# Optimization experiments

Measured on AMD Instinct MI355X. Metric: run time of the kernel, lower is better.

The kernel has to match this reference:

```python
import jax, jax.numpy as jnp
import numpy as np

N_NODES = 100000
N_EDGES = 1600000
IN_DIM, HID_DIM, OUT_DIM = 128, 128, 64


def setup_inputs() -> dict:
    key = jax.random.key(0)
    k1, k2, k3, k4 = jax.random.split(key, 4)
    x = jax.random.normal(k1, (N_NODES, IN_DIM), dtype=jnp.float32)
    edge_index = jax.random.randint(k2, (2, N_EDGES), 0, N_NODES, dtype=jnp.int64)
    W1 = jax.random.normal(k3, (IN_DIM, HID_DIM), dtype=jnp.float32) * (1.0 / np.sqrt(IN_DIM))
    b1 = jnp.zeros((HID_DIM,), dtype=jnp.float32)
    W2 = jax.random.normal(k4, (HID_DIM, OUT_DIM), dtype=jnp.float32) * (1.0 / np.sqrt(HID_DIM))
    b2 = jnp.zeros((OUT_DIM,), dtype=jnp.float32)
    return {"x": x, "edge_index": edge_index, "W1": W1, "b1": b1, "W2": W2, "b2": b2}


def _gcn_conv(x, W, b, src, dst, num_nodes):
    # PyG GCNConv (normalize=True): h = D^{-1/2} A_hat D^{-1/2} (x W) + b
    h = x @ W  # [N, out]
    ones = jnp.ones(src.shape[0], dtype=h.dtype)
    deg = jax.ops.segment_sum(ones, dst, num_segments=num_nodes)  # in-degree incl self-loops
    dinv = jnp.where(deg > 0, jax.lax.rsqrt(deg), jnp.zeros_like(deg))
    norm = dinv[src] * dinv[dst]  # [E]
    msg = h[src] * norm[:, None]  # gather + scale, [E, out]
    out = jax.ops.segment_sum(msg, dst, num_segments=num_nodes)  # scatter-add
    return out + b


def reference(x, edge_index, W1, b1, W2, b2):
    n = x.shape[0]
    loop = jnp.arange(n, dtype=edge_index.dtype)
    src = jnp.concatenate([edge_index[0], loop])  # add_self_loops=True
    dst = jnp.concatenate([edge_index[1], loop])
    h = jax.nn.elu(_gcn_conv(x, W1, b1, src, dst, n))
    out = jax.nn.elu(_gcn_conv(h, W2, b2, src, dst, n))
    return out
```

## Files before the change

kernel.cpp:

```cpp
#include <hip/hip_runtime.h>
#include <hip/hip_bf16.h>

#define N_NODES 100000
#define N_EDGES 1600000
#define IN_DIM  128
#define HID_DIM 128
#define OUT_DIM 64

#define BKT_BITS 9
#define BKT_SIZE 512
#define NBUCK    ((N_NODES + BKT_SIZE - 1) / BKT_SIZE)
#define BCAP     8768
#define EPB      2048
#define NTILE    8

typedef __attribute__((ext_vector_type(8))) short short8;
typedef __attribute__((ext_vector_type(4))) float floatx4;

__device__ __forceinline__ float eluf(float x) { return x > 0.0f ? x : expm1f(x); }
__device__ __forceinline__ unsigned short bfbits(float f) {
    union { __hip_bfloat16 h; unsigned short u; } c; c.h = __float2bfloat16(f); return c.u;
}
__device__ __forceinline__ unsigned packbf(float a, float b) {
    return (unsigned)bfbits(a) | ((unsigned)bfbits(b) << 16);
}
__device__ __forceinline__ float lo16(unsigned u) { return __uint_as_float(u << 16); }
__device__ __forceinline__ float hi16(unsigned u) { return __uint_as_float(u & 0xffff0000u); }
__device__ __forceinline__ unsigned tile_of(unsigned src) { return (src * 8u) / 100000u; }

__device__ __forceinline__ int esrc(const int* ei, int e, int is64) {
    return is64 ? ei[2 * e] : ei[e];
}
__device__ __forceinline__ int edst(const int* ei, int e, int is64) {
    return is64 ? ei[2 * (N_EDGES + e)] : ei[N_EDGES + e];
}

__global__ void k_init(const int* __restrict__ ei, int* __restrict__ flag,
                       int* __restrict__ cursor) {
    __shared__ int acc;
    if (threadIdx.x == 0) acc = 0;
    __syncthreads();
    int v = 0;
    for (int e = threadIdx.x; e < 1024; e += 256) v |= ei[2 * e + 1];
    atomicOr(&acc, v);
    __syncthreads();
    if (threadIdx.x == 0) flag[0] = (acc == 0) ? 1 : 0;
    if (threadIdx.x < NBUCK) cursor[threadIdx.x] = 0;
}

__launch_bounds__(256)
__global__ void k_bucket(const int* __restrict__ ei, const int* __restrict__ flag,
                         int* __restrict__ cursor, unsigned* __restrict__ eb) {
    __shared__ int hist[NBUCK];
    __shared__ int base[NBUCK];
    int t = threadIdx.x;
    int is64 = flag[0];
    int e0 = blockIdx.x * EPB;
    int s[8], d[8];
#pragma unroll
    for (int q = 0; q < 8; q++) {
        int e = e0 + q * 256 + t;
        if (e < N_EDGES) { s[q] = esrc(ei, e, is64); d[q] = edst(ei, e, is64); }
        else d[q] = -1;
    }
    for (int i = t; i < NBUCK; i += 256) hist[i] = 0;
    __syncthreads();
#pragma unroll
    for (int q = 0; q < 8; q++)
        if (d[q] >= 0) atomicAdd(&hist[d[q] >> BKT_BITS], 1);
    __syncthreads();
    for (int i = t; i < NBUCK; i += 256) {
        int h = hist[i];
        base[i] = (h > 0) ? atomicAdd(&cursor[i], h) : 0;
    }
    __syncthreads();
#pragma unroll
    for (int q = 0; q < 8; q++)
        if (d[q] >= 0) {
            int bk = d[q] >> BKT_BITS;
            int p = atomicAdd(&base[bk], 1);
            if (p < BCAP)
                eb[bk * BCAP + p] = ((unsigned)s[q] << BKT_BITS) | (unsigned)(d[q] & (BKT_SIZE - 1));
        }
}

__launch_bounds__(256)
__global__ void k_csr(const int* __restrict__ cursor, unsigned* __restrict__ eb,
                      unsigned short* __restrict__ row16, unsigned char* __restrict__ deg8,
                      float* __restrict__ dinv) {
    __shared__ unsigned stage[BCAP];
    __shared__ int bins[BKT_SIZE * NTILE];
    __shared__ int sc[256];
    int t = threadIdx.x, b = blockIdx.x;
    int cbeg = b * BCAP;
    int count = cursor[b];
    if (count > BCAP) count = BCAP;
    for (int i = t; i < BKT_SIZE * NTILE; i += 256) bins[i] = 0;
    __syncthreads();
    for (int i = t; i < count; i += 256) {
        unsigned e = eb[cbeg + i];
        stage[i] = e;
        unsigned key = ((e & (BKT_SIZE - 1)) << 3) + tile_of(e >> BKT_BITS);
        atomicAdd(&bins[key], 1);
    }
    __syncthreads();
    int loc[16];
    int s = 0;
#pragma unroll
    for (int i = 0; i < 16; i++) { loc[i] = bins[t * 16 + i]; s += loc[i]; }
    sc[t] = s;
    __syncthreads();
    int acc = s;
    for (int off = 1; off < 256; off <<= 1) {
        int v = (t >= off) ? sc[t - off] : 0;
        __syncthreads();
        acc += v; sc[t] = acc;
        __syncthreads();
    }
    int run = acc - s;
#pragma unroll
    for (int i = 0; i < 16; i++) { bins[t * 16 + i] = run; run += loc[i]; }
    __syncthreads();
    int nbase = b * BKT_SIZE;
    for (int i = t; i < BKT_SIZE; i += 256) {
        int n = nbase + i;
        if (n < N_NODES) {
            int st = bins[i << 3];
            int en = (i == BKT_SIZE - 1) ? count : bins[(i + 1) << 3];
            row16[n] = (unsigned short)st;
            deg8[n] = (unsigned char)(en - st);
            dinv[n] = rsqrtf((float)(en - st) + 1.0f);
        }
    }
    __syncthreads();
    for (int i = t; i < count; i += 256) {
        unsigned e = stage[i];
        unsigned src = e >> BKT_BITS;
        unsigned key = ((e & (BKT_SIZE - 1)) << 3) + tile_of(src);
        int p = atomicAdd(&bins[key], 1);
        eb[cbeg + p] = src;
    }
}

__global__ void k_cast_scale(const float4* __restrict__ x4, const float* __restrict__ dinv,
                             uint2* __restrict__ xbs) {
    int i = blockIdx.x * blockDim.x + threadIdx.x;
    if (i >= N_NODES * (IN_DIM / 4)) return;
    float dd = dinv[i >> 5];
    float4 v = x4[i];
    uint2 o = { packbf(v.x * dd, v.y * dd), packbf(v.z * dd, v.w * dd) };
    xbs[i] = o;
}

__launch_bounds__(256)
__global__ void k_gather1(const unsigned* __restrict__ xbs, const float* __restrict__ dinv,
                          const unsigned short* __restrict__ row16,
                          const unsigned char* __restrict__ deg8,
                          const unsigned* __restrict__ csr, unsigned* __restrict__ agg) {
    int w = (blockIdx.x * blockDim.x + threadIdx.x) >> 6;
    int lane = threadIdx.x & 63;
    if (w >= N_NODES) return;
    int beg = (w >> BKT_BITS) * BCAP + row16[w];
    int dg = deg8[w];
    beg = __builtin_amdgcn_readfirstlane(beg);
    int end = beg + __builtin_amdgcn_readfirstlane(dg);
    float dd = dinv[w];
    unsigned sv = xbs[w * 64 + lane];
    float a0 = lo16(sv), a1 = hi16(sv);
    int j = beg;
    for (; j + 8 <= end; j += 8) {
        int s[8]; unsigned u[8];
#pragma unroll
        for (int q = 0; q < 8; q++) s[q] = (int)csr[j + q];
#pragma unroll
        for (int q = 0; q < 8; q++) u[q] = xbs[s[q] * 64 + lane];
#pragma unroll
        for (int q = 0; q < 8; q++) { a0 += lo16(u[q]); a1 += hi16(u[q]); }
    }
    if (j + 4 <= end) {
        int s[4]; unsigned u[4];
#pragma unroll
        for (int q = 0; q < 4; q++) s[q] = (int)csr[j + q];
#pragma unroll
        for (int q = 0; q < 4; q++) u[q] = xbs[s[q] * 64 + lane];
#pragma unroll
        for (int q = 0; q < 4; q++) { a0 += lo16(u[q]); a1 += hi16(u[q]); }
        j += 4;
    }
    if (j + 2 <= end) {
        int s0 = (int)csr[j], s1 = (int)csr[j + 1];
        unsigned u0 = xbs[s0 * 64 + lane], u1 = xbs[s1 * 64 + lane];
        a0 += lo16(u0) + lo16(u1); a1 += hi16(u0) + hi16(u1);
        j += 2;
    }
    if (j < end) {
        unsigned u0 = xbs[(int)csr[j] * 64 + lane];
        a0 += lo16(u0); a1 += hi16(u0);
    }
    agg[w * 64 + lane] = packbf(a0 * dd, a1 * dd);
}

__launch_bounds__(256)
__global__ void k_gather2(const unsigned* __restrict__ h2s, const float* __restrict__ dinv,
                          const unsigned short* __restrict__ row16,
                          const unsigned char* __restrict__ deg8,
                          const unsigned* __restrict__ csr,
                          const float* __restrict__ b2, float2* __restrict__ out) {
    int w = (blockIdx.x * blockDim.x + threadIdx.x) >> 6;
    int lane = threadIdx.x & 63;
    if (w >= N_NODES) return;
    int half = lane >> 5, p = lane & 31;
    int beg = (w >> BKT_BITS) * BCAP + row16[w];
    int dg = deg8[w];
    beg = __builtin_amdgcn_readfirstlane(beg);
    int end = beg + __builtin_amdgcn_readfirstlane(dg);
    float dd = dinv[w];
    unsigned sv = h2s[w * 32 + p];
    float a0 = half ? 0.0f : lo16(sv);
    float a1 = half ? 0.0f : hi16(sv);
    int j = beg;
    for (; j + 8 <= end; j += 8) {
        int s[8]; unsigned u[4];
#pragma unroll
        for (int q = 0; q < 8; q++) s[q] = (int)csr[j + q];
#pragma unroll
        for (int i = 0; i < 4; i++) u[i] = h2s[s[2 * i + half] * 32 + p];
#pragma unroll
        for (int i = 0; i < 4; i++) { a0 += lo16(u[i]); a1 += hi16(u[i]); }
    }
    if (j + 4 <= end) {
        int s[4];
#pragma unroll
        for (int q = 0; q < 4; q++) s[q] = (int)csr[j + q];
        unsigned u0 = h2s[s[half] * 32 + p];
        unsigned u1 = h2s[s[2 + half] * 32 + p];
        a0 += lo16(u0) + lo16(u1); a1 += hi16(u0) + hi16(u1);
        j += 4;
    }
    if (j + 2 <= end) {
        int s0 = (int)csr[j], s1 = (int)csr[j + 1];
        unsigned u = h2s[(half ? s1 : s0) * 32 + p];
        a0 += lo16(u); a1 += hi16(u);
        j += 2;
    }
    if (j < end && !half) {
        unsigned u = h2s[(int)csr[j] * 32 + p];
        a0 += lo16(u); a1 += hi16(u);
    }
    a0 += __shfl_xor(a0, 32);
    a1 += __shfl_xor(a1, 32);
    if (!half) {
        float2 bias = *(const float2*)(b2 + 2 * p);
        float2 r = { eluf(a0 * dd + bias.x), eluf(a1 * dd + bias.y) };
        out[w * 32 + p] = r;
    }
}

__launch_bounds__(256)
__global__ void k_gemm1_mfma(unsigned* __restrict__ agg, const float* __restrict__ W1,
                             const float* __restrict__ b1, int nblk) {
    __shared__ short w1p[4][8][64][8];
    int t = threadIdx.x;
    for (int idx = t; idx < 8192; idx += 256) {
        int j2 = idx & 3, l = (idx >> 2) & 63, ct = (idx >> 8) & 7, kk = idx >> 11;
        int k = kk * 32 + (l >> 4) * 8 + j2 * 2;
        int c = ct * 16 + (l & 15);
        ((unsigned*)w1p)[idx] = packbf(W1[k * HID_DIM + c], W1[(k + 1) * HID_DIM + c]);
    }
    int lane = t & 63, wave = t >> 6;
    int q = lane >> 4, m = lane & 15;
    floatx4 bias[8];
#pragma unroll
    for (int ct = 0; ct < 8; ct++) bias[ct] = *(const floatx4*)(b1 + ct * 16 + q * 4);
    __syncthreads();
    for (int blk = blockIdx.x * 4 + wave; blk < nblk; blk += gridDim.x * 4) {
        int r = blk * 16 + m;
        const short8* arow = (const short8*)(agg + r * 64);
        short8 bfr[4];
#pragma unroll
        for (int kk = 0; kk < 4; kk++) bfr[kk] = arow[kk * 4 + q];
        floatx4 acc[8];
#pragma unroll
        for (int ct = 0; ct < 8; ct++) acc[ct] = (floatx4)0.0f;
#pragma unroll
        for (int kk = 0; kk < 4; kk++)
#pragma unroll
            for (int ct = 0; ct < 8; ct++) {
                short8 af = *(const short8*)(&w1p[kk][ct][lane][0]);
                acc[ct] = __builtin_amdgcn_mfma_f32_16x16x32_bf16(af, bfr[kk], acc[ct], 0, 0, 0);
            }
        unsigned* hrow = agg + r * 64;
#pragma unroll
        for (int ct = 0; ct < 8; ct++) {
            uint2 o;
            o.x = packbf(eluf(acc[ct][0] + bias[ct][0]), eluf(acc[ct][1] + bias[ct][1]));
            o.y = packbf(eluf(acc[ct][2] + bias[ct][2]), eluf(acc[ct][3] + bias[ct][3]));
            *(uint2*)(hrow + ct * 8 + q * 2) = o;
        }
    }
}

__launch_bounds__(256)
__global__ void k_gemm2_mfma(const unsigned* __restrict__ h1, const float* __restrict__ W2,
                             const float* __restrict__ dinv, unsigned* __restrict__ h2s,
                             int nblk) {
    __shared__ short w2p[4][4][64][8];
    int t = threadIdx.x;
    for (int idx = t; idx < 4096; idx += 256) {
        int j2 = idx & 3, l = (idx >> 2) & 63, ct = (idx >> 8) & 3, kk = idx >> 10;
        int k = kk * 32 + (l >> 4) * 8 + j2 * 2;
        int c = ct * 16 + (l & 15);
        ((unsigned*)w2p)[idx] = packbf(W2[k * OUT_DIM + c], W2[(k + 1) * OUT_DIM + c]);
    }
    int lane = t & 63, wave = t >> 6;
    int q = lane >> 4, m = lane & 15;
    __syncthreads();
    for (int blk = blockIdx.x * 4 + wave; blk < nblk; blk += gridDim.x * 4) {
        int r = blk * 16 + m;
        const short8* arow = (const short8*)(h1 + r * 64);
        short8 bfr[4];
#pragma unroll
        for (int kk = 0; kk < 4; kk++) bfr[kk] = arow[kk * 4 + q];
        floatx4 acc[4];
#pragma unroll
        for (int ct = 0; ct < 4; ct++) acc[ct] = (floatx4)0.0f;
#pragma unroll
        for (int kk = 0; kk < 4; kk++)
#pragma unroll
            for (int ct = 0; ct < 4; ct++) {
                short8 af = *(const short8*)(&w2p[kk][ct][lane][0]);
                acc[ct] = __builtin_amdgcn_mfma_f32_16x16x32_bf16(af, bfr[kk], acc[ct], 0, 0, 0);
            }
        float ddr = dinv[r];
        unsigned* orow = h2s + r * 32;
#pragma unroll
        for (int ct = 0; ct < 4; ct++) {
            uint2 o;
            o.x = packbf(acc[ct][0] * ddr, acc[ct][1] * ddr);
            o.y = packbf(acc[ct][2] * ddr, acc[ct][3] * ddr);
            *(uint2*)(orow + ct * 8 + q * 2) = o;
        }
    }
}

extern "C" void kernel_launch(void* const* d_in, const int* in_sizes, int n_in,
                              void* d_out, int out_size, void* d_ws, size_t ws_size,
                              hipStream_t stream) {
    const float* x  = (const float*)d_in[0];
    const int*   ei = (const int*)d_in[1];
    const float* W1 = (const float*)d_in[2];
    const float* b1 = (const float*)d_in[3];
    const float* W2 = (const float*)d_in[4];
    const float* b2 = (const float*)d_in[5];

    const size_t OFF_FLAG  = 0;
    const size_t OFF_CUR   = 16;
    const size_t OFF_ROW16 = 272;
    const size_t OFF_DEG8  = 50272;
    const size_t OFF_DINV  = 75272;
    const size_t OFF_EB    = 175272;
    const size_t OFF_XB    = 1893800;
    const size_t OFF_AGG   = 8293800;
    const size_t needed = (OFF_AGG + 6400000) * 4;
    if (ws_size < needed) return;

    int*            flag   = (int*)d_ws + OFF_FLAG;
    int*            cursor = (int*)d_ws + OFF_CUR;
    unsigned short* row16  = (unsigned short*)((int*)d_ws + OFF_ROW16);
    unsigned char*  deg8   = (unsigned char*)((int*)d_ws + OFF_DEG8);
    float*          dinv   = (float*)d_ws + OFF_DINV;
    unsigned*       eb     = (unsigned*)d_ws + OFF_EB;
    unsigned*       xbs    = (unsigned*)d_ws + OFF_XB;
    unsigned*       agg    = (unsigned*)d_ws + OFF_AGG;

    k_init<<<1, 256, 0, stream>>>(ei, flag, cursor);
    k_bucket<<<(N_EDGES + EPB - 1) / EPB, 256, 0, stream>>>(ei, flag, cursor, eb);
    k_csr<<<NBUCK, 256, 0, stream>>>(cursor, eb, row16, deg8, dinv);

    k_cast_scale<<<(N_NODES * (IN_DIM / 4) + 255) / 256, 256, 0, stream>>>(
        (const float4*)x, dinv, (uint2*)xbs);

    k_gather1<<<(N_NODES * 64 + 255) / 256, 256, 0, stream>>>(
        xbs, dinv, row16, deg8, eb, agg);
    k_gemm1_mfma<<<1024, 256, 0, stream>>>(agg, W1, b1, N_NODES / 16);

    k_gemm2_mfma<<<1024, 256, 0, stream>>>(agg, W2, dinv, xbs, N_NODES / 16);
    k_gather2<<<(N_NODES * 64 + 255) / 256, 256, 0, stream>>>(
        xbs, dinv, row16, deg8, eb, b2, (float2*)d_out);
}
```

Before: 327.2 us.

## Tile-synchronised multi-node gather, fuse both GEMMs, prepack weights once

```diff
diff --git a/kernel.cpp b/kernel.cpp
--- a/kernel.cpp
+++ b/kernel.cpp
@@ -14,6 +14,9 @@
 #define EPB      2048
 #define NTILE    8
 
+#define G1B 1536
+#define NPW 17
+
 typedef __attribute__((ext_vector_type(8))) short short8;
 typedef __attribute__((ext_vector_type(4))) float floatx4;
 
@@ -36,16 +39,37 @@
 }
 
 __global__ void k_init(const int* __restrict__ ei, int* __restrict__ flag,
-                       int* __restrict__ cursor) {
+                       int* __restrict__ cursor, const float* __restrict__ W1,
+                       const float* __restrict__ W2, unsigned* __restrict__ w1q,
+                       unsigned* __restrict__ w2q) {
+    int t = threadIdx.x;
+    if (blockIdx.x == 1) {
+        for (int idx = t; idx < 8192; idx += 256) {
+            int j2 = idx & 3, l = (idx >> 2) & 63, ct = (idx >> 8) & 7, kk = idx >> 11;
+            int k = kk * 32 + (l >> 4) * 8 + j2 * 2;
+            int c = ct * 16 + (l & 15);
+            w1q[idx] = packbf(W1[k * HID_DIM + c], W1[(k + 1) * HID_DIM + c]);
+        }
+        return;
+    }
+    if (blockIdx.x == 2) {
+        for (int idx = t; idx < 4096; idx += 256) {
+            int j2 = idx & 3, l = (idx >> 2) & 63, ct = (idx >> 8) & 3, kk = idx >> 10;
+            int k = kk * 32 + (l >> 4) * 8 + j2 * 2;
+            int c = ct * 16 + (l & 15);
+            w2q[idx] = packbf(W2[k * OUT_DIM + c], W2[(k + 1) * OUT_DIM + c]);
+        }
+        return;
+    }
     __shared__ int acc;
-    if (threadIdx.x == 0) acc = 0;
+    if (t == 0) acc = 0;
     __syncthreads();
     int v = 0;
-    for (int e = threadIdx.x; e < 1024; e += 256) v |= ei[2 * e + 1];
+    for (int e = t; e < 1024; e += 256) v |= ei[2 * e + 1];
     atomicOr(&acc, v);
     __syncthreads();
-    if (threadIdx.x == 0) flag[0] = (acc == 0) ? 1 : 0;
-    if (threadIdx.x < NBUCK) cursor[threadIdx.x] = 0;
+    if (t == 0) flag[0] = (acc == 0) ? 1 : 0;
+    if (t < NBUCK) cursor[t] = 0;
 }
 
 __launch_bounds__(256)
@@ -87,7 +111,7 @@
 __launch_bounds__(256)
 __global__ void k_csr(const int* __restrict__ cursor, unsigned* __restrict__ eb,
                       unsigned short* __restrict__ row16, unsigned char* __restrict__ deg8,
-                      float* __restrict__ dinv) {
+                      float* __restrict__ dinv, unsigned short* __restrict__ ts16) {
     __shared__ unsigned stage[BCAP];
     __shared__ int bins[BKT_SIZE * NTILE];
     __shared__ int sc[256];
@@ -130,6 +154,12 @@
             row16[n] = (unsigned short)st;
             deg8[n] = (unsigned char)(en - st);
             dinv[n] = rsqrtf((float)(en - st) + 1.0f);
+            uint4 o;
+            o.x = (unsigned)bins[i * 8 + 0] | ((unsigned)bins[i * 8 + 1] << 16);
+            o.y = (unsigned)bins[i * 8 + 2] | ((unsigned)bins[i * 8 + 3] << 16);
+            o.z = (unsigned)bins[i * 8 + 4] | ((unsigned)bins[i * 8 + 5] << 16);
+            o.w = (unsigned)bins[i * 8 + 6] | ((unsigned)bins[i * 8 + 7] << 16);
+            ((uint4*)ts16)[n] = o;
         }
     }
     __syncthreads();
@@ -152,52 +182,138 @@
     xbs[i] = o;
 }
 
+__launch_bounds__(256, 6)
+__global__ void k_gather1_ts(const unsigned* __restrict__ xbs,
+                             const float* __restrict__ dinv,
+                             const unsigned char* __restrict__ deg8,
+                             const unsigned short* __restrict__ ts16,
+                             const unsigned* __restrict__ csr,
+                             unsigned* __restrict__ agg) {
+    int tid = threadIdx.x;
+    int wid = __builtin_amdgcn_readfirstlane((int)(blockIdx.x * 256 + tid) >> 6);
+    int lane = tid & 63;
+    int n0 = wid * NPW;
+    float a0[NPW], a1[NPW];
+#pragma unroll
+    for (int i = 0; i < NPW; i++) { a0[i] = 0.0f; a1[i] = 0.0f; }
+    for (int t = 0; t < 8; t++) {
+#pragma unroll
+        for (int i = 0; i < NPW; i++) {
+            int n = n0 + i;
+            if (n < N_NODES) {
+                int bb = (n >> BKT_BITS) * BCAP;
+                int a = bb + (int)ts16[n * 8 + t];
+                int b = (t < 7) ? bb + (int)ts16[n * 8 + t + 1]
+                                : bb + (int)ts16[n * 8] + (int)deg8[n];
+                a = __builtin_amdgcn_readfirstlane(a);
+                b = __builtin_amdgcn_readfirstlane(b);
+                if ((int)tile_of((unsigned)n) == t) {
+                    unsigned u = xbs[n * 64 + lane];
+                    a0[i] += lo16(u); a1[i] += hi16(u);
+                }
+                while (a + 4 <= b) {
+                    int s0 = __builtin_amdgcn_readfirstlane((int)csr[a]);
+                    int s1 = __builtin_amdgcn_readfirstlane((int)csr[a + 1]);
+                    int s2 = __builtin_amdgcn_readfirstlane((int)csr[a + 2]);
+                    int s3 = __builtin_amdgcn_readfirstlane((int)csr[a + 3]);
+                    unsigned u0 = xbs[s0 * 64 + lane], u1 = xbs[s1 * 64 + lane];
+                    unsigned u2 = xbs[s2 * 64 + lane], u3 = xbs[s3 * 64 + lane];
+                    a0[i] += lo16(u0) + lo16(u1) + lo16(u2) + lo16(u3);
+                    a1[i] += hi16(u0) + hi16(u1) + hi16(u2) + hi16(u3);
+                    a += 4;
+                }
+                if (a + 2 <= b) {
+                    int s0 = __builtin_amdgcn_readfirstlane((int)csr[a]);
+                    int s1 = __builtin_amdgcn_readfirstlane((int)csr[a + 1]);
+                    unsigned u0 = xbs[s0 * 64 + lane], u1 = xbs[s1 * 64 + lane];
+                    a0[i] += lo16(u0) + lo16(u1);
+                    a1[i] += hi16(u0) + hi16(u1);
+                    a += 2;
+                }
+                if (a < b) {
+                    int s0 = __builtin_amdgcn_readfirstlane((int)csr[a]);
+                    unsigned u0 = xbs[s0 * 64 + lane];
+                    a0[i] += lo16(u0); a1[i] += hi16(u0);
+                }
+            }
+        }
+        __syncthreads();
+    }
+#pragma unroll
+    for (int i = 0; i < NPW; i++) {
+        int n = n0 + i;
+        if (n < N_NODES) {
+            float dd = dinv[n];
+            agg[n * 64 + lane] = packbf(a0[i] * dd, a1[i] * dd);
+        }
+    }
+}
+
 __launch_bounds__(256)
-__global__ void k_gather1(const unsigned* __restrict__ xbs, const float* __restrict__ dinv,
-                          const unsigned short* __restrict__ row16,
-                          const unsigned char* __restrict__ deg8,
-                          const unsigned* __restrict__ csr, unsigned* __restrict__ agg) {
-    int w = (blockIdx.x * blockDim.x + threadIdx.x) >> 6;
-    int lane = threadIdx.x & 63;
-    if (w >= N_NODES) return;
-    int beg = (w >> BKT_BITS) * BCAP + row16[w];
-    int dg = deg8[w];
-    beg = __builtin_amdgcn_readfirstlane(beg);
-    int end = beg + __builtin_amdgcn_readfirstlane(dg);
-    float dd = dinv[w];
-    unsigned sv = xbs[w * 64 + lane];
-    float a0 = lo16(sv), a1 = hi16(sv);
-    int j = beg;
-    for (; j + 8 <= end; j += 8) {
-        int s[8]; unsigned u[8];
-#pragma unroll
-        for (int q = 0; q < 8; q++) s[q] = (int)csr[j + q];
-#pragma unroll
-        for (int q = 0; q < 8; q++) u[q] = xbs[s[q] * 64 + lane];
-#pragma unroll
-        for (int q = 0; q < 8; q++) { a0 += lo16(u[q]); a1 += hi16(u[q]); }
-    }
-    if (j + 4 <= end) {
-        int s[4]; unsigned u[4];
-#pragma unroll
-        for (int q = 0; q < 4; q++) s[q] = (int)csr[j + q];
-#pragma unroll
-        for (int q = 0; q < 4; q++) u[q] = xbs[s[q] * 64 + lane];
-#pragma unroll
-        for (int q = 0; q < 4; q++) { a0 += lo16(u[q]); a1 += hi16(u[q]); }
-        j += 4;
-    }
-    if (j + 2 <= end) {
-        int s0 = (int)csr[j], s1 = (int)csr[j + 1];
-        unsigned u0 = xbs[s0 * 64 + lane], u1 = xbs[s1 * 64 + lane];
-        a0 += lo16(u0) + lo16(u1); a1 += hi16(u0) + hi16(u1);
-        j += 2;
-    }
-    if (j < end) {
-        unsigned u0 = xbs[(int)csr[j] * 64 + lane];
-        a0 += lo16(u0); a1 += hi16(u0);
-    }
-    agg[w * 64 + lane] = packbf(a0 * dd, a1 * dd);
+__global__ void k_gemm12(const unsigned* __restrict__ agg, const unsigned* __restrict__ w1q,
+                         const unsigned* __restrict__ w2q, const float* __restrict__ b1,
+                         const float* __restrict__ dinv, unsigned* __restrict__ h2s,
+                         int nblk) {
+    __shared__ unsigned w1p[8192];
+    __shared__ unsigned w2p[4096];
+    __shared__ unsigned h1s[4][16 * 68 + 4];
+    int t = threadIdx.x;
+    for (int i = t; i < 8192; i += 256) w1p[i] = w1q[i];
+    for (int i = t; i < 4096; i += 256) w2p[i] = w2q[i];
+    int lane = t & 63, wave = t >> 6;
+    int q = lane >> 4, m = lane & 15;
+    floatx4 bias[8];
+#pragma unroll
+    for (int ct = 0; ct < 8; ct++) bias[ct] = *(const floatx4*)(b1 + ct * 16 + q * 4);
+    __syncthreads();
+    unsigned* hst = &h1s[wave][0];
+    for (int blk = blockIdx.x * 4 + wave; blk < nblk; blk += gridDim.x * 4) {
+        int r = blk * 16 + m;
+        const short8* arow = (const short8*)(agg + r * 64);
+        short8 bfr[4];
+#pragma unroll
+        for (int kk = 0; kk < 4; kk++) bfr[kk] = arow[kk * 4 + q];
+        floatx4 acc[8];
+#pragma unroll
+        for (int ct = 0; ct < 8; ct++) acc[ct] = (floatx4)0.0f;
+#pragma unroll
+        for (int kk = 0; kk < 4; kk++)
+#pragma unroll
+            for (int ct = 0; ct < 8; ct++) {
+                short8 af = *(const short8*)(w1p + ((kk * 8 + ct) * 64 + lane) * 4);
+                acc[ct] = __builtin_amdgcn_mfma_f32_16x16x32_bf16(af, bfr[kk], acc[ct], 0, 0, 0);
+            }
+#pragma unroll
+        for (int ct = 0; ct < 8; ct++) {
+            uint2 o;
+            o.x = packbf(eluf(acc[ct][0] + bias[ct][0]), eluf(acc[ct][1] + bias[ct][1]));
+            o.y = packbf(eluf(acc[ct][2] + bias[ct][2]), eluf(acc[ct][3] + bias[ct][3]));
+            *(uint2*)(hst + m * 68 + ct * 8 + q * 2) = o;
+        }
+        short8 bfr2[4];
+#pragma unroll
+        for (int kk = 0; kk < 4; kk++)
+            bfr2[kk] = *(const short8*)(hst + m * 68 + (kk * 4 + q) * 4);
+        floatx4 acc2[4];
+#pragma unroll
+        for (int ct = 0; ct < 4; ct++) acc2[ct] = (floatx4)0.0f;
+#pragma unroll
+        for (int kk = 0; kk < 4; kk++)
+#pragma unroll
+            for (int ct = 0; ct < 4; ct++) {
+                short8 af = *(const short8*)(w2p + ((kk * 4 + ct) * 64 + lane) * 4);
+                acc2[ct] = __builtin_amdgcn_mfma_f32_16x16x32_bf16(af, bfr2[kk], acc2[ct], 0, 0, 0);
+            }
+        float ddr = dinv[r];
+        unsigned* orow = h2s + r * 32;
+#pragma unroll
+        for (int ct = 0; ct < 4; ct++) {
+            uint2 o;
+            o.x = packbf(acc2[ct][0] * ddr, acc2[ct][1] * ddr);
+            o.y = packbf(acc2[ct][2] * ddr, acc2[ct][3] * ddr);
+            *(uint2*)(orow + ct * 8 + q * 2) = o;
+        }
+    }
 }
 
 __launch_bounds__(256)
@@ -256,93 +372,6 @@
     }
 }
 
-__launch_bounds__(256)
-__global__ void k_gemm1_mfma(unsigned* __restrict__ agg, const float* __restrict__ W1,
-                             const float* __restrict__ b1, int nblk) {
-    __shared__ short w1p[4][8][64][8];
-    int t = threadIdx.x;
-    for (int idx = t; idx < 8192; idx += 256) {
-        int j2 = idx & 3, l = (idx >> 2) & 63, ct = (idx >> 8) & 7, kk = idx >> 11;
-        int k = kk * 32 + (l >> 4) * 8 + j2 * 2;
-        int c = ct * 16 + (l & 15);
-        ((unsigned*)w1p)[idx] = packbf(W1[k * HID_DIM + c], W1[(k + 1) * HID_DIM + c]);
-    }
-    int lane = t & 63, wave = t >> 6;
-    int q = lane >> 4, m = lane & 15;
-    floatx4 bias[8];
-#pragma unroll
-    for (int ct = 0; ct < 8; ct++) bias[ct] = *(const floatx4*)(b1 + ct * 16 + q * 4);
-    __syncthreads();
-    for (int blk = blockIdx.x * 4 + wave; blk < nblk; blk += gridDim.x * 4) {
-        int r = blk * 16 + m;
-        const short8* arow = (const short8*)(agg + r * 64);
-        short8 bfr[4];
-#pragma unroll
-        for (int kk = 0; kk < 4; kk++) bfr[kk] = arow[kk * 4 + q];
-        floatx4 acc[8];
-#pragma unroll
-        for (int ct = 0; ct < 8; ct++) acc[ct] = (floatx4)0.0f;
-#pragma unroll
-        for (int kk = 0; kk < 4; kk++)
-#pragma unroll
-            for (int ct = 0; ct < 8; ct++) {
-                short8 af = *(const short8*)(&w1p[kk][ct][lane][0]);
-                acc[ct] = __builtin_amdgcn_mfma_f32_16x16x32_bf16(af, bfr[kk], acc[ct], 0, 0, 0);
-            }
-        unsigned* hrow = agg + r * 64;
-#pragma unroll
-        for (int ct = 0; ct < 8; ct++) {
-            uint2 o;
-            o.x = packbf(eluf(acc[ct][0] + bias[ct][0]), eluf(acc[ct][1] + bias[ct][1]));
-            o.y = packbf(eluf(acc[ct][2] + bias[ct][2]), eluf(acc[ct][3] + bias[ct][3]));
-            *(uint2*)(hrow + ct * 8 + q * 2) = o;
-        }
-    }
-}
-
-__launch_bounds__(256)
-__global__ void k_gemm2_mfma(const unsigned* __restrict__ h1, const float* __restrict__ W2,
-                             const float* __restrict__ dinv, unsigned* __restrict__ h2s,
-                             int nblk) {
-    __shared__ short w2p[4][4][64][8];
-    int t = threadIdx.x;
-    for (int idx = t; idx < 4096; idx += 256) {
-        int j2 = idx & 3, l = (idx >> 2) & 63, ct = (idx >> 8) & 3, kk = idx >> 10;
-        int k = kk * 32 + (l >> 4) * 8 + j2 * 2;
-        int c = ct * 16 + (l & 15);
-        ((unsigned*)w2p)[idx] = packbf(W2[k * OUT_DIM + c], W2[(k + 1) * OUT_DIM + c]);
-    }
-    int lane = t & 63, wave = t >> 6;
-    int q = lane >> 4, m = lane & 15;
-    __syncthreads();
-    for (int blk = blockIdx.x * 4 + wave; blk < nblk; blk += gridDim.x * 4) {
-        int r = blk * 16 + m;
-        const short8* arow = (const short8*)(h1 + r * 64);
-        short8 bfr[4];
-#pragma unroll
-        for (int kk = 0; kk < 4; kk++) bfr[kk] = arow[kk * 4 + q];
-        floatx4 acc[4];
-#pragma unroll
-        for (int ct = 0; ct < 4; ct++) acc[ct] = (floatx4)0.0f;
-#pragma unroll
-        for (int kk = 0; kk < 4; kk++)
-#pragma unroll
-            for (int ct = 0; ct < 4; ct++) {
-                short8 af = *(const short8*)(&w2p[kk][ct][lane][0]);
-                acc[ct] = __builtin_amdgcn_mfma_f32_16x16x32_bf16(af, bfr[kk], acc[ct], 0, 0, 0);
-            }
-        float ddr = dinv[r];
-        unsigned* orow = h2s + r * 32;
-#pragma unroll
-        for (int ct = 0; ct < 4; ct++) {
-            uint2 o;
-            o.x = packbf(acc[ct][0] * ddr, acc[ct][1] * ddr);
-            o.y = packbf(acc[ct][2] * ddr, acc[ct][3] * ddr);
-            *(uint2*)(orow + ct * 8 + q * 2) = o;
-        }
-    }
-}
-
 extern "C" void kernel_launch(void* const* d_in, const int* in_sizes, int n_in,
                               void* d_out, int out_size, void* d_ws, size_t ws_size,
                               hipStream_t stream) {
@@ -373,18 +402,21 @@
     unsigned*       xbs    = (unsigned*)d_ws + OFF_XB;
     unsigned*       agg    = (unsigned*)d_ws + OFF_AGG;
 
-    k_init<<<1, 256, 0, stream>>>(ei, flag, cursor);
+    unsigned short* ts16 = (unsigned short*)d_out;
+    unsigned*       w1q  = (unsigned*)d_out + 400000;
+    unsigned*       w2q  = (unsigned*)d_out + 408192;
+
+    k_init<<<3, 256, 0, stream>>>(ei, flag, cursor, W1, W2, w1q, w2q);
     k_bucket<<<(N_EDGES + EPB - 1) / EPB, 256, 0, stream>>>(ei, flag, cursor, eb);
-    k_csr<<<NBUCK, 256, 0, stream>>>(cursor, eb, row16, deg8, dinv);
+    k_csr<<<NBUCK, 256, 0, stream>>>(cursor, eb, row16, deg8, dinv, ts16);
 
     k_cast_scale<<<(N_NODES * (IN_DIM / 4) + 255) / 256, 256, 0, stream>>>(
         (const float4*)x, dinv, (uint2*)xbs);
 
-    k_gather1<<<(N_NODES * 64 + 255) / 256, 256, 0, stream>>>(
-        xbs, dinv, row16, deg8, eb, agg);
-    k_gemm1_mfma<<<1024, 256, 0, stream>>>(agg, W1, b1, N_NODES / 16);
-
-    k_gemm2_mfma<<<1024, 256, 0, stream>>>(agg, W2, dinv, xbs, N_NODES / 16);
+    k_gather1_ts<<<G1B, 256, 0, stream>>>(xbs, dinv, deg8, ts16, eb, agg);
+
+    k_gemm12<<<512, 256, 0, stream>>>(agg, w1q, w2q, b1, dinv, xbs, N_NODES / 16);
+
     k_gather2<<<(N_NODES * 64 + 255) / 256, 256, 0, stream>>>(
         xbs, dinv, row16, deg8, eb, b2, (float2*)d_out);
 }
```

Result: slower. 454.7 us (+38.9%).

## Fuse both GEMMs via LDS, prepack weights, drop tile sort in CSR build

Applied to the files above, without the earlier changes.

```diff
diff --git a/kernel.cpp b/kernel.cpp
--- a/kernel.cpp
+++ b/kernel.cpp
@@ -12,7 +12,6 @@
 #define NBUCK    ((N_NODES + BKT_SIZE - 1) / BKT_SIZE)
 #define BCAP     8768
 #define EPB      2048
-#define NTILE    8
 
 typedef __attribute__((ext_vector_type(8))) short short8;
 typedef __attribute__((ext_vector_type(4))) float floatx4;
@@ -26,7 +25,6 @@
 }
 __device__ __forceinline__ float lo16(unsigned u) { return __uint_as_float(u << 16); }
 __device__ __forceinline__ float hi16(unsigned u) { return __uint_as_float(u & 0xffff0000u); }
-__device__ __forceinline__ unsigned tile_of(unsigned src) { return (src * 8u) / 100000u; }
 
 __device__ __forceinline__ int esrc(const int* ei, int e, int is64) {
     return is64 ? ei[2 * e] : ei[e];
@@ -36,16 +34,37 @@
 }
 
 __global__ void k_init(const int* __restrict__ ei, int* __restrict__ flag,
-                       int* __restrict__ cursor) {
+                       int* __restrict__ cursor, const float* __restrict__ W1,
+                       const float* __restrict__ W2, unsigned* __restrict__ w1q,
+                       unsigned* __restrict__ w2q) {
+    int t = threadIdx.x;
+    if (blockIdx.x == 1) {
+        for (int idx = t; idx < 8192; idx += 256) {
+            int j2 = idx & 3, l = (idx >> 2) & 63, ct = (idx >> 8) & 7, kk = idx >> 11;
+            int k = kk * 32 + (l >> 4) * 8 + j2 * 2;
+            int c = ct * 16 + (l & 15);
+            w1q[idx] = packbf(W1[k * HID_DIM + c], W1[(k + 1) * HID_DIM + c]);
+        }
+        return;
+    }
+    if (blockIdx.x == 2) {
+        for (int idx = t; idx < 4096; idx += 256) {
+            int j2 = idx & 3, l = (idx >> 2) & 63, ct = (idx >> 8) & 3, kk = idx >> 10;
+            int k = kk * 32 + (l >> 4) * 8 + j2 * 2;
+            int c = ct * 16 + (l & 15);
+            w2q[idx] = packbf(W2[k * OUT_DIM + c], W2[(k + 1) * OUT_DIM + c]);
+        }
+        return;
+    }
     __shared__ int acc;
-    if (threadIdx.x == 0) acc = 0;
+    if (t == 0) acc = 0;
     __syncthreads();
     int v = 0;
-    for (int e = threadIdx.x; e < 1024; e += 256) v |= ei[2 * e + 1];
+    for (int e = t; e < 1024; e += 256) v |= ei[2 * e + 1];
     atomicOr(&acc, v);
     __syncthreads();
-    if (threadIdx.x == 0) flag[0] = (acc == 0) ? 1 : 0;
-    if (threadIdx.x < NBUCK) cursor[threadIdx.x] = 0;
+    if (t == 0) flag[0] = (acc == 0) ? 1 : 0;
+    if (t < NBUCK) cursor[t] = 0;
 }
 
 __launch_bounds__(256)
@@ -84,61 +103,55 @@
         }
 }
 
-__launch_bounds__(256)
+__launch_bounds__(1024)
 __global__ void k_csr(const int* __restrict__ cursor, unsigned* __restrict__ eb,
                       unsigned short* __restrict__ row16, unsigned char* __restrict__ deg8,
                       float* __restrict__ dinv) {
     __shared__ unsigned stage[BCAP];
-    __shared__ int bins[BKT_SIZE * NTILE];
+    __shared__ int bins[BKT_SIZE];
+    __shared__ int cur[BKT_SIZE];
     __shared__ int sc[256];
     int t = threadIdx.x, b = blockIdx.x;
     int cbeg = b * BCAP;
     int count = cursor[b];
     if (count > BCAP) count = BCAP;
-    for (int i = t; i < BKT_SIZE * NTILE; i += 256) bins[i] = 0;
-    __syncthreads();
-    for (int i = t; i < count; i += 256) {
+    if (t < BKT_SIZE) bins[t] = 0;
+    __syncthreads();
+    for (int i = t; i < count; i += 1024) {
         unsigned e = eb[cbeg + i];
         stage[i] = e;
-        unsigned key = ((e & (BKT_SIZE - 1)) << 3) + tile_of(e >> BKT_BITS);
-        atomicAdd(&bins[key], 1);
-    }
-    __syncthreads();
-    int loc[16];
-    int s = 0;
-#pragma unroll
-    for (int i = 0; i < 16; i++) { loc[i] = bins[t * 16 + i]; s += loc[i]; }
-    sc[t] = s;
+        atomicAdd(&bins[e & (BKT_SIZE - 1)], 1);
+    }
+    __syncthreads();
+    int h0 = 0, h1 = 0, s = 0;
+    if (t < 256) { h0 = bins[2 * t]; h1 = bins[2 * t + 1]; s = h0 + h1; sc[t] = s; }
     __syncthreads();
     int acc = s;
     for (int off = 1; off < 256; off <<= 1) {
-        int v = (t >= off) ? sc[t - off] : 0;
+        int v = (t >= off && t < 256) ? sc[t - off] : 0;
         __syncthreads();
-        acc += v; sc[t] = acc;
+        if (t < 256) { acc += v; sc[t] = acc; }
         __syncthreads();
     }
-    int run = acc - s;
-#pragma unroll
-    for (int i = 0; i < 16; i++) { bins[t * 16 + i] = run; run += loc[i]; }
-    __syncthreads();
-    int nbase = b * BKT_SIZE;
-    for (int i = t; i < BKT_SIZE; i += 256) {
-        int n = nbase + i;
+    if (t < 256) {
+        int ex = acc - s;
+        cur[2 * t] = ex;
+        cur[2 * t + 1] = ex + h0;
+    }
+    __syncthreads();
+    if (t < BKT_SIZE) {
+        int n = b * BKT_SIZE + t;
         if (n < N_NODES) {
-            int st = bins[i << 3];
-            int en = (i == BKT_SIZE - 1) ? count : bins[(i + 1) << 3];
-            row16[n] = (unsigned short)st;
-            deg8[n] = (unsigned char)(en - st);
-            dinv[n] = rsqrtf((float)(en - st) + 1.0f);
-        }
-    }
-    __syncthreads();
-    for (int i = t; i < count; i += 256) {
+            row16[n] = (unsigned short)cur[t];
+            deg8[n] = (unsigned char)bins[t];
+            dinv[n] = rsqrtf((float)bins[t] + 1.0f);
+        }
+    }
+    __syncthreads();
+    for (int i = t; i < count; i += 1024) {
         unsigned e = stage[i];
-        unsigned src = e >> BKT_BITS;
-        unsigned key = ((e & (BKT_SIZE - 1)) << 3) + tile_of(src);
-        int p = atomicAdd(&bins[key], 1);
-        eb[cbeg + p] = src;
+        int p = atomicAdd(&cur[e & (BKT_SIZE - 1)], 1);
+        eb[cbeg + p] = e >> BKT_BITS;
     }
 }
 
@@ -198,6 +211,73 @@
         a0 += lo16(u0); a1 += hi16(u0);
     }
     agg[w * 64 + lane] = packbf(a0 * dd, a1 * dd);
+}
+
+__launch_bounds__(256)
+__global__ void k_gemm12(const unsigned* __restrict__ agg, const unsigned* __restrict__ w1q,
+                         const unsigned* __restrict__ w2q, const float* __restrict__ b1,
+                         const float* __restrict__ dinv, unsigned* __restrict__ h2s,
+                         int nblk) {
+    __shared__ unsigned w1p[8192];
+    __shared__ unsigned w2p[4096];
+    __shared__ unsigned h1s[4][16 * 68 + 4];
+    int t = threadIdx.x;
+    for (int i = t; i < 8192; i += 256) w1p[i] = w1q[i];
+    for (int i = t; i < 4096; i += 256) w2p[i] = w2q[i];
+    int lane = t & 63, wave = t >> 6;
+    int q = lane >> 4, m = lane & 15;
+    floatx4 bias[8];
+#pragma unroll
+    for (int ct = 0; ct < 8; ct++) bias[ct] = *(const floatx4*)(b1 + ct * 16 + q * 4);
+    __syncthreads();
+    unsigned* hst = &h1s[wave][0];
+    for (int blk = blockIdx.x * 4 + wave; blk < nblk; blk += gridDim.x * 4) {
+        int r = blk * 16 + m;
+        const short8* arow = (const short8*)(agg + r * 64);
+        short8 bfr[4];
+#pragma unroll
+        for (int kk = 0; kk < 4; kk++) bfr[kk] = arow[kk * 4 + q];
+        floatx4 acc[8];
+#pragma unroll
+        for (int ct = 0; ct < 8; ct++) acc[ct] = (floatx4)0.0f;
+#pragma unroll
+        for (int kk = 0; kk < 4; kk++)
+#pragma unroll
+            for (int ct = 0; ct < 8; ct++) {
+                short8 af = *(const short8*)(w1p + ((kk * 8 + ct) * 64 + lane) * 4);
+                acc[ct] = __builtin_amdgcn_mfma_f32_16x16x32_bf16(af, bfr[kk], acc[ct], 0, 0, 0);
+            }
+#pragma unroll
+        for (int ct = 0; ct < 8; ct++) {
+            uint2 o;
+            o.x = packbf(eluf(acc[ct][0] + bias[ct][0]), eluf(acc[ct][1] + bias[ct][1]));
+            o.y = packbf(eluf(acc[ct][2] + bias[ct][2]), eluf(acc[ct][3] + bias[ct][3]));
+            *(uint2*)(hst + m * 68 + ct * 8 + q * 2) = o;
+        }
+        short8 bfr2[4];
+#pragma unroll
+        for (int kk = 0; kk < 4; kk++)
+            bfr2[kk] = *(const short8*)(hst + m * 68 + (kk * 4 + q) * 4);
+        floatx4 acc2[4];
+#pragma unroll
+        for (int ct = 0; ct < 4; ct++) acc2[ct] = (floatx4)0.0f;
+#pragma unroll
+        for (int kk = 0; kk < 4; kk++)
+#pragma unroll
+            for (int ct = 0; ct < 4; ct++) {
+                short8 af = *(const short8*)(w2p + ((kk * 4 + ct) * 64 + lane) * 4);
+                acc2[ct] = __builtin_amdgcn_mfma_f32_16x16x32_bf16(af, bfr2[kk], acc2[ct], 0, 0, 0);
+            }
+        float ddr = dinv[r];
+        unsigned* orow = h2s + r * 32;
+#pragma unroll
+        for (int ct = 0; ct < 4; ct++) {
+            uint2 o;
+            o.x = packbf(acc2[ct][0] * ddr, acc2[ct][1] * ddr);
+            o.y = packbf(acc2[ct][2] * ddr, acc2[ct][3] * ddr);
+            *(uint2*)(orow + ct * 8 + q * 2) = o;
+        }
+    }
 }
 
 __launch_bounds__(256)
@@ -256,93 +336,6 @@
     }
 }
 
-__launch_bounds__(256)
-__global__ void k_gemm1_mfma(unsigned* __restrict__ agg, const float* __restrict__ W1,
-                             const float* __restrict__ b1, int nblk) {
-    __shared__ short w1p[4][8][64][8];
-    int t = threadIdx.x;
-    for (int idx = t; idx < 8192; idx += 256) {
-        int j2 = idx & 3, l = (idx >> 2) & 63, ct = (idx >> 8) & 7, kk = idx >> 11;
-        int k = kk * 32 + (l >> 4) * 8 + j2 * 2;
-        int c = ct * 16 + (l & 15);
-        ((unsigned*)w1p)[idx] = packbf(W1[k * HID_DIM + c], W1[(k + 1) * HID_DIM + c]);
-    }
-    int lane = t & 63, wave = t >> 6;
-    int q = lane >> 4, m = lane & 15;
-    floatx4 bias[8];
-#pragma unroll
-    for (int ct = 0; ct < 8; ct++) bias[ct] = *(const floatx4*)(b1 + ct * 16 + q * 4);
-    __syncthreads();
-    for (int blk = blockIdx.x * 4 + wave; blk < nblk; blk += gridDim.x * 4) {
-        int r = blk * 16 + m;
-        const short8* arow = (const short8*)(agg + r * 64);
-        short8 bfr[4];
-#pragma unroll
-        for (int kk = 0; kk < 4; kk++) bfr[kk] = arow[kk * 4 + q];
-        floatx4 acc[8];
-#pragma unroll
-        for (int ct = 0; ct < 8; ct++) acc[ct] = (floatx4)0.0f;
-#pragma unroll
-        for (int kk = 0; kk < 4; kk++)
-#pragma unroll
-            for (int ct = 0; ct < 8; ct++) {
-                short8 af = *(const short8*)(&w1p[kk][ct][lane][0]);
-                acc[ct] = __builtin_amdgcn_mfma_f32_16x16x32_bf16(af, bfr[kk], acc[ct], 0, 0, 0);
-            }
-        unsigned* hrow = agg + r * 64;
-#pragma unroll
-        for (int ct = 0; ct < 8; ct++) {
-            uint2 o;
-            o.x = packbf(eluf(acc[ct][0] + bias[ct][0]), eluf(acc[ct][1] + bias[ct][1]));
-            o.y = packbf(eluf(acc[ct][2] + bias[ct][2]), eluf(acc[ct][3] + bias[ct][3]));
-            *(uint2*)(hrow + ct * 8 + q * 2) = o;
-        }
-    }
-}
-
-__launch_bounds__(256)
-__global__ void k_gemm2_mfma(const unsigned* __restrict__ h1, const float* __restrict__ W2,
-                             const float* __restrict__ dinv, unsigned* __restrict__ h2s,
-                             int nblk) {
-    __shared__ short w2p[4][4][64][8];
-    int t = threadIdx.x;
-    for (int idx = t; idx < 4096; idx += 256) {
-        int j2 = idx & 3, l = (idx >> 2) & 63, ct = (idx >> 8) & 3, kk = idx >> 10;
-        int k = kk * 32 + (l >> 4) * 8 + j2 * 2;
-        int c = ct * 16 + (l & 15);
-        ((unsigned*)w2p)[idx] = packbf(W2[k * OUT_DIM + c], W2[(k + 1) * OUT_DIM + c]);
-    }
-    int lane = t & 63, wave = t >> 6;
-    int q = lane >> 4, m = lane & 15;
-    __syncthreads();
-    for (int blk = blockIdx.x * 4 + wave; blk < nblk; blk += gridDim.x * 4) {
-        int r = blk * 16 + m;
-        const short8* arow = (const short8*)(h1 + r * 64);
-        short8 bfr[4];
-#pragma unroll
-        for (int kk = 0; kk < 4; kk++) bfr[kk] = arow[kk * 4 + q];
-        floatx4 acc[4];
-#pragma unroll
-        for (int ct = 0; ct < 4; ct++) acc[ct] = (floatx4)0.0f;
-#pragma unroll
-        for (int kk = 0; kk < 4; kk++)
-#pragma unroll
-            for (int ct = 0; ct < 4; ct++) {
-                short8 af = *(const short8*)(&w2p[kk][ct][lane][0]);
-                acc[ct] = __builtin_amdgcn_mfma_f32_16x16x32_bf16(af, bfr[kk], acc[ct], 0, 0, 0);
-            }
-        float ddr = dinv[r];
-        unsigned* orow = h2s + r * 32;
-#pragma unroll
-        for (int ct = 0; ct < 4; ct++) {
-            uint2 o;
-            o.x = packbf(acc[ct][0] * ddr, acc[ct][1] * ddr);
-            o.y = packbf(acc[ct][2] * ddr, acc[ct][3] * ddr);
-            *(uint2*)(orow + ct * 8 + q * 2) = o;
-        }
-    }
-}
-
 extern "C" void kernel_launch(void* const* d_in, const int* in_sizes, int n_in,
                               void* d_out, int out_size, void* d_ws, size_t ws_size,
                               hipStream_t stream) {
@@ -373,18 +366,21 @@
     unsigned*       xbs    = (unsigned*)d_ws + OFF_XB;
     unsigned*       agg    = (unsigned*)d_ws + OFF_AGG;
 
-    k_init<<<1, 256, 0, stream>>>(ei, flag, cursor);
+    unsigned* w1q = (unsigned*)d_out;
+    unsigned* w2q = (unsigned*)d_out + 8192;
+
+    k_init<<<3, 256, 0, stream>>>(ei, flag, cursor, W1, W2, w1q, w2q);
     k_bucket<<<(N_EDGES + EPB - 1) / EPB, 256, 0, stream>>>(ei, flag, cursor, eb);
-    k_csr<<<NBUCK, 256, 0, stream>>>(cursor, eb, row16, deg8, dinv);
+    k_csr<<<NBUCK, 1024, 0, stream>>>(cursor, eb, row16, deg8, dinv);
 
     k_cast_scale<<<(N_NODES * (IN_DIM / 4) + 255) / 256, 256, 0, stream>>>(
         (const float4*)x, dinv, (uint2*)xbs);
 
     k_gather1<<<(N_NODES * 64 + 255) / 256, 256, 0, stream>>>(
         xbs, dinv, row16, deg8, eb, agg);
-    k_gemm1_mfma<<<1024, 256, 0, stream>>>(agg, W1, b1, N_NODES / 16);
-
-    k_gemm2_mfma<<<1024, 256, 0, stream>>>(agg, W2, dinv, xbs, N_NODES / 16);
+
+    k_gemm12<<<512, 256, 0, stream>>>(agg, w1q, w2q, b1, dinv, xbs, N_NODES / 16);
+
     k_gather2<<<(N_NODES * 64 + 255) / 256, 256, 0, stream>>>(
         xbs, dinv, row16, deg8, eb, b2, (float2*)d_out);
 }
```

Measured after the change: 320.3 us, median of 2. 1.02x faster.
